# Performance work log

Measured on AMD Instinct MI355X. Metric: run time of the kernel, lower is better.

## Reference

```python
import jax, jax.numpy as jnp
import numpy as np

L, B, S, D, H = 6, 2, 2048, 512, 8
DH = D // H
FF = 4 * D
EPS = 1e-5


def setup_inputs() -> dict:
    key = jax.random.key(0)
    ks = jax.random.split(key, 10)
    w = lambda k, shape: jax.random.normal(k, shape, jnp.float32) * 0.02
    return {
        "query": jax.random.normal(ks[0], (B, S, D), jnp.float32),
        "key": jax.random.normal(ks[1], (B, S, D), jnp.float32),
        "query_mask": jnp.ones((B, S), jnp.int32),
        "key_mask": jnp.ones((B, S), jnp.int32),
        # per-layer stacked params; conv1d(kernel=1) == linear with weight [out,in]
        "Wq": w(ks[2], (L, D, D)), "bq": jnp.zeros((L, D), jnp.float32),
        "Wk": w(ks[3], (L, D, D)), "bk": jnp.zeros((L, D), jnp.float32),
        "Wv": w(ks[4], (L, D, D)), "bv": jnp.zeros((L, D), jnp.float32),
        "Wo": w(ks[5], (L, D, D)), "bo": jnp.zeros((L, D), jnp.float32),
        "ln1_g": jnp.ones((L, D), jnp.float32), "ln1_b": jnp.zeros((L, D), jnp.float32),
        "ff_w1": w(ks[6], (L, FF, D)), "ff_b1": jnp.zeros((L, FF), jnp.float32),
        "ff_w2": w(ks[7], (L, D, FF)), "ff_b2": jnp.zeros((L, D), jnp.float32),
        "ln2_g": jnp.ones((L, D), jnp.float32), "ln2_b": jnp.zeros((L, D), jnp.float32),
    }


def _layer_norm(x, g, b):
    m = jnp.mean(x, axis=-1, keepdims=True)
    v = jnp.mean(jnp.square(x - m), axis=-1, keepdims=True)
    return (x - m) * jax.lax.rsqrt(v + EPS) * g + b


def reference(query, key, query_mask, key_mask,
              Wq, bq, Wk, bk, Wv, bv, Wo, bo,
              ln1_g, ln1_b, ff_w1, ff_b1, ff_w2, ff_b2, ln2_g, ln2_b):
    b_, s_, d_ = query.shape
    kpad = (key_mask == 0)[:, None, None, :]          # [B,1,1,K]
    qm = query_mask.astype(query.dtype)[:, :, None]    # [B,S,1]
    x = query
    for i in range(L):
        # QKV projections (conv1d kernel-size-1 == linear), split heads -> [B,H,S,DH]
        def split(t):
            return t.reshape(b_, s_, H, DH).transpose(0, 2, 1, 3)
        q = split(x @ Wq[i].T + bq[i]) * (float(DH) ** -0.5)
        k = split(key @ Wk[i].T + bk[i])
        v = split(key @ Wv[i].T + bv[i])
        attn = jnp.einsum('bhqd,bhkd->bhqk', q, k)
        attn = jnp.where(kpad, -jnp.inf, attn)
        attn = jax.nn.softmax(attn, axis=-1)
        o = jnp.einsum('bhqk,bhkd->bhqd', attn, v)
        o = o.transpose(0, 2, 1, 3).reshape(b_, s_, H * DH)
        o = (o @ Wo[i].T + bo[i]) * qm                 # output proj + query mask
        x = _layer_norm(o + x, ln1_g[i], ln1_b[i])
        h = jax.nn.leaky_relu(x @ ff_w1[i].T + ff_b1[i], 0.01)
        f = (h @ ff_w2[i].T + ff_b2[i]) * qm           # FFN mask on output
        x = _layer_norm(f + x, ln2_g[i], ln2_b[i])
    return x
```

## Files before the change

### kernel.cpp

```cpp
#include <hip/hip_runtime.h>
#include <stdint.h>

constexpr int LAYERS = 6;
constexpr int Bc = 2, Sc = 2048, Dc = 512, Hc = 8, DHc = 64, FFc = 2048;
constexpr int Mc = Bc * Sc;
constexpr int NS = 2;
constexpr int KCHUNK = Sc / NS;

typedef __attribute__((ext_vector_type(8))) __bf16 bf16x8;
typedef __attribute__((ext_vector_type(4))) __bf16 bf16x4;
typedef __attribute__((ext_vector_type(4))) float f32x4;

__device__ __forceinline__ void async_ld16(const void* g, void* lds) {
  __builtin_amdgcn_global_load_lds(
      (const __attribute__((address_space(1))) uint32_t*)g,
      (__attribute__((address_space(3))) uint32_t*)lds, 16, 0, 0);
}

__global__ __launch_bounds__(256) void cvt_kernel(const float* __restrict__ in,
                                                  __bf16* __restrict__ out, int n) {
  int i = (blockIdx.x * 256 + threadIdx.x) * 4;
  if (i + 4 > n) return;
  const float4 v = *(const float4*)(in + i);
  bf16x4 o;
  o[0] = (__bf16)v.x; o[1] = (__bf16)v.y; o[2] = (__bf16)v.z; o[3] = (__bf16)v.w;
  *(bf16x4*)(out + i) = o;
}

__global__ __launch_bounds__(256) void cvt_kv_kernel(const float* __restrict__ Wk,
                                                     const float* __restrict__ Wv,
                                                     __bf16* __restrict__ out) {
  size_t i = ((size_t)blockIdx.x * 256 + threadIdx.x) * 4;
  int n = (int)(i / ((size_t)Dc * Dc));
  int lyr = n >> 1, p = n & 1;
  size_t idx = i - (size_t)n * Dc * Dc;
  const float* src = (p ? Wv : Wk) + (size_t)lyr * Dc * Dc + idx;
  const float4 v = *(const float4*)src;
  bf16x4 o;
  o[0] = (__bf16)v.x; o[1] = (__bf16)v.y; o[2] = (__bf16)v.z; o[3] = (__bf16)v.w;
  *(bf16x4*)(out + i) = o;
}

__global__ __launch_bounds__(256) void kbias_kernel(const int* __restrict__ km,
                                                    float* __restrict__ kb, int n) {
  int i = blockIdx.x * 256 + threadIdx.x;
  if (i < n) kb[i] = km[i] ? 0.f : -1e30f;
}

template <int BM, int BN, int WM, int WN, int EPI>
__global__ __launch_bounds__(256) void gemm_bt(
    const __bf16* __restrict__ A, const __bf16* __restrict__ W,
    const float* __restrict__ bias, const float* __restrict__ bias2,
    float* __restrict__ outf, __bf16* __restrict__ outb,
    __bf16* __restrict__ outb2, float scale,
    int M, int N, int K, int Kstride) {
  constexpr int BK = 64;
  __shared__ __bf16 As[2][BM * BK];
  __shared__ __bf16 Bs[2][BN * BK];
  const int tid = threadIdx.x;
  const int l15 = tid & 15;
  const int lg = (tid & 63) >> 4;
  const int w = tid >> 6;
  const int wm = w >> 1, wn = w & 1;
  const int tm = blockIdx.y * BM;
  const int tn = blockIdx.x * BN;
  const int z = blockIdx.z;
  const __bf16* Ap = A + (size_t)tm * Kstride + (size_t)z * K;
  const __bf16* Wp = W + (size_t)tn * Kstride + (size_t)z * K;
  f32x4 acc[WM][WN] = {};

  auto stage = [&](int k0, int bf) {
#pragma unroll
    for (int c = 0; c < BM * 8 / 256; ++c) {
      int cc = c * 256 + tid;
      int r = cc >> 3, s = cc & 7;
      int ss = s ^ (r & 7);
      async_ld16(Ap + (size_t)r * Kstride + k0 + ss * 8, &As[bf][cc * 8]);
    }
#pragma unroll
    for (int c = 0; c < BN * 8 / 256; ++c) {
      int cc = c * 256 + tid;
      int r = cc >> 3, s = cc & 7;
      int ss = s ^ (r & 7);
      async_ld16(Wp + (size_t)r * Kstride + k0 + ss * 8, &Bs[bf][cc * 8]);
    }
  };

  const int nk = K / BK;
  stage(0, 0);
  __syncthreads();
  int buf = 0;
  for (int t = 0; t < nk; ++t) {
    if (t + 1 < nk) stage((t + 1) * BK, buf ^ 1);
    bf16x8 af[WM][2], bfr[WN][2];
#pragma unroll
    for (int i = 0; i < WM; ++i) {
      int row = wm * WM * 16 + i * 16 + l15;
#pragma unroll
      for (int kf = 0; kf < 2; ++kf)
        af[i][kf] = *(const bf16x8*)&As[buf][row * 64 + (((kf * 4 + lg) ^ (row & 7)) * 8)];
    }
#pragma unroll
    for (int j = 0; j < WN; ++j) {
      int row = wn * WN * 16 + j * 16 + l15;
#pragma unroll
      for (int kf = 0; kf < 2; ++kf)
        bfr[j][kf] = *(const bf16x8*)&Bs[buf][row * 64 + (((kf * 4 + lg) ^ (row & 7)) * 8)];
    }
#pragma unroll
    for (int kf = 0; kf < 2; ++kf)
#pragma unroll
      for (int i = 0; i < WM; ++i)
#pragma unroll
        for (int j = 0; j < WN; ++j)
          acc[i][j] = __builtin_amdgcn_mfma_f32_16x16x32_bf16(af[i][kf], bfr[j][kf], acc[i][j], 0, 0, 0);
    __syncthreads();
    buf ^= 1;
  }

  if constexpr (EPI == 6) {
    const bool isV = ((tn & 1023) >= 512);
    const int lyr = tn >> 10;
    const int b = tm >> 11;
    const int sbase = tm & (Sc - 1);
    if (isV) {
      __bf16* T = (__bf16*)&As[0][0];
#pragma unroll
      for (int i = 0; i < WM; ++i) {
#pragma unroll
        for (int j = 0; j < WN; ++j) {
          const int d = wn * WN * 16 + j * 16 + l15;
          const int dg = (tn & 511) + d;
          const float bv = bias2[lyr * 512 + dg];
          const int s0 = wm * WM * 16 + i * 16 + lg * 4;
          bf16x4 pk;
#pragma unroll
          for (int r = 0; r < 4; ++r) pk[r] = (__bf16)(acc[i][j][r] + bv);
          const int slot = (s0 >> 3) ^ (d & 7);
          *(bf16x4*)&T[d * 64 + slot * 8 + (s0 & 7)] = pk;
        }
      }
      __syncthreads();
      const int rr = tid >> 3;
      const int c8 = tid & 7;
#pragma unroll
      for (int pass = 0; pass < 4; ++pass) {
        const int d = pass * 32 + rr;
        const int slot = c8 ^ (d & 7);
        bf16x8 v8 = *(const bf16x8*)&T[d * 64 + slot * 8];
        const int dg = (tn & 511) + d;
        const int h = dg >> 6, dh = dg & 63;
        *(bf16x8*)&outb2[((((size_t)(lyr * Bc + b) * Hc + h)) * DHc + dh) * Sc +
                         sbase + c8 * 8] = v8;
      }
    } else {
#pragma unroll
      for (int i = 0; i < WM; ++i) {
#pragma unroll
        for (int j = 0; j < WN; ++j) {
          const int d = wn * WN * 16 + j * 16 + l15;
          const int dg = (tn & 511) + d;
          const float bv = bias[lyr * 512 + dg];
          const int h = dg >> 6, dh = dg & 63;
#pragma unroll
          for (int r = 0; r < 4; ++r) {
            const int s = sbase + wm * WM * 16 + i * 16 + lg * 4 + r;
            outb[((((size_t)(lyr * Bc + b) * Hc + h)) * Sc + s) * DHc + dh] =
                (__bf16)(acc[i][j][r] + bv);
          }
        }
      }
    }
    return;
  }

#pragma unroll
  for (int i = 0; i < WM; ++i) {
#pragma unroll
    for (int j = 0; j < WN; ++j) {
      const int n = tn + wn * WN * 16 + j * 16 + l15;
      float bv;
      if constexpr (EPI == 0) {
        bv = (z == 0) ? bias[n] : 0.f;
      } else {
        bv = bias[n];
      }
#pragma unroll
      for (int r = 0; r < 4; ++r) {
        const int m = tm + wm * WM * 16 + i * 16 + lg * 4 + r;
        float v = acc[i][j][r] + bv;
        if constexpr (EPI == 0) {
          outf[(size_t)z * M * N + (size_t)m * N + n] = v;
        } else if constexpr (EPI == 1) {
          int b = m >> 11, s = m & (Sc - 1);
          int h = n >> 6, dh = n & 63;
          outb[(((size_t)(b * Hc + h)) * Sc + s) * DHc + dh] = (__bf16)(v * scale);
        } else if constexpr (EPI == 4) {
          float lv = v > 0.f ? v : 0.01f * v;
          outb[(size_t)m * N + n] = (__bf16)lv;
        }
      }
    }
  }
}

__global__ __launch_bounds__(256, 5) void attn_kernel(
    const __bf16* __restrict__ q, const __bf16* __restrict__ k,
    const __bf16* __restrict__ vt, const float* __restrict__ kb,
    __bf16* __restrict__ Opart, float* __restrict__ mpart,
    float* __restrict__ lpart) {
  const int bid = blockIdx.x;
  const int o = (bid & 7) * 128 + (bid >> 3);
  const int qb = o & 31;
  const int p = o >> 5;
  const int bh = p >> 1;
  const int z = p & 1;
  const int b = bh >> 3;
  const int w = threadIdx.x >> 6;
  const int l = threadIdx.x & 63;
  const int l15 = l & 15;
  const int lg = l >> 4;
  const int tid = threadIdx.x;
  const int qbase = qb * 64 + w * 16;
  const int k0 = z * KCHUNK;

  const __bf16* qp = q + ((size_t)bh * Sc + qbase) * DHc;
  const __bf16* kp = k + (size_t)bh * Sc * DHc;
  const __bf16* vp = vt + (size_t)bh * DHc * Sc;
  const float* kbp = kb + (size_t)b * Sc;

  bf16x8 qf[2];
  qf[0] = *(const bf16x8*)(qp + l15 * DHc + lg * 8);
  qf[1] = *(const bf16x8*)(qp + l15 * DHc + 32 + lg * 8);

  bf16x8 onesf;
#pragma unroll
  for (int i = 0; i < 8; ++i) onesf[i] = (__bf16)1.0f;

  f32x4 oacc[4] = {};
  f32x4 lacc = {};
  float mr = -1e30f;

  __shared__ __bf16 Ks[2][4096];
  __shared__ __bf16 Vs[2][4096];

  auto stage = [&](int t, int bf) {
    const int kt = k0 + t * 64;
#pragma unroll
    for (int ii = 0; ii < 2; ++ii) {
      int i = ii * 256 + tid;
      int r = i >> 3;
      int bsrc = (i & 7) ^ (r & 7);
      async_ld16(kp + (size_t)(kt + r) * DHc + bsrc * 8, &Ks[bf][i * 8]);
      async_ld16(vp + (size_t)r * Sc + kt + bsrc * 8, &Vs[bf][i * 8]);
    }
  };

  stage(0, 0);
  __syncthreads();

  constexpr int NT = KCHUNK / 64;
  int buf = 0;
  for (int t = 0; t < NT; ++t) {
    const int kt = k0 + t * 64;
    if (t + 1 < NT) stage(t + 1, buf ^ 1);

    float4 mb4[4];
#pragma unroll
    for (int cb = 0; cb < 4; ++cb)
      mb4[cb] = *(const float4*)&kbp[kt + cb * 16 + lg * 4];

    f32x4 sacc[4] = {};
#pragma unroll
    for (int kf = 0; kf < 2; ++kf) {
#pragma unroll
      for (int cb = 0; cb < 4; ++cb) {
        int row = cb * 16 + l15;
        bf16x8 kfr = *(const bf16x8*)&Ks[buf][row * 64 + (((kf * 4 + lg) ^ (row & 7)) * 8)];
        sacc[cb] = __builtin_amdgcn_mfma_f32_16x16x32_bf16(kfr, qf[kf], sacc[cb], 0, 0, 0);
      }
    }
    sacc[0][0] += mb4[0].x; sacc[0][1] += mb4[0].y; sacc[0][2] += mb4[0].z; sacc[0][3] += mb4[0].w;
    sacc[1][0] += mb4[1].x; sacc[1][1] += mb4[1].y; sacc[1][2] += mb4[1].z; sacc[1][3] += mb4[1].w;
    sacc[2][0] += mb4[2].x; sacc[2][1] += mb4[2].y; sacc[2][2] += mb4[2].z; sacc[2][3] += mb4[2].w;
    sacc[3][0] += mb4[3].x; sacc[3][1] += mb4[3].y; sacc[3][2] += mb4[3].z; sacc[3][3] += mb4[3].w;

    float mx = sacc[0][0];
#pragma unroll
    for (int cb = 0; cb < 4; ++cb)
#pragma unroll
      for (int r = 0; r < 4; ++r) mx = fmaxf(mx, sacc[cb][r]);
    mx = fmaxf(mx, __shfl_xor(mx, 16, 64));
    mx = fmaxf(mx, __shfl_xor(mx, 32, 64));

    if (__any(mx > mr + 8.f)) {
      float mn = fmaxf(mr, mx);
      float f = __expf(mr - mn);
      mr = mn;
      float fj[4];
#pragma unroll
      for (int j = 0; j < 4; ++j) fj[j] = __shfl(f, lg * 4 + j, 64);
#pragma unroll
      for (int j = 0; j < 4; ++j) lacc[j] *= fj[j];
#pragma unroll
      for (int db = 0; db < 4; ++db)
#pragma unroll
        for (int j = 0; j < 4; ++j) oacc[db][j] *= fj[j];
    }

    unsigned pw[4][2];
#pragma unroll
    for (int cb = 0; cb < 4; ++cb) {
#pragma unroll
      for (int w2 = 0; w2 < 2; ++w2) {
        union { __bf16 h[2]; unsigned u; } cu;
        cu.h[0] = (__bf16)__expf(sacc[cb][2 * w2] - mr);
        cu.h[1] = (__bf16)__expf(sacc[cb][2 * w2 + 1] - mr);
        pw[cb][w2] = cu.u;
      }
    }

    const int srcA = ((lg & 1) * 2) * 16 + l15;
    const int srcB = srcA + 16;
    const bool hi = (lg >> 1) & 1;
#pragma unroll
    for (int kf = 0; kf < 2; ++kf) {
      unsigned t0a = __shfl((int)pw[kf * 2][0], srcA, 64);
      unsigned t0b = __shfl((int)pw[kf * 2 + 1][0], srcA, 64);
      unsigned t1a = __shfl((int)pw[kf * 2][1], srcA, 64);
      unsigned t1b = __shfl((int)pw[kf * 2 + 1][1], srcA, 64);
      unsigned t2a = __shfl((int)pw[kf * 2][0], srcB, 64);
      unsigned t2b = __shfl((int)pw[kf * 2 + 1][0], srcB, 64);
      unsigned t3a = __shfl((int)pw[kf * 2][1], srcB, 64);
      unsigned t3b = __shfl((int)pw[kf * 2 + 1][1], srcB, 64);
      union { unsigned u[4]; bf16x8 v; } pa;
      pa.u[0] = hi ? t0b : t0a;
      pa.u[1] = hi ? t1b : t1a;
      pa.u[2] = hi ? t2b : t2a;
      pa.u[3] = hi ? t3b : t3a;
      lacc = __builtin_amdgcn_mfma_f32_16x16x32_bf16(pa.v, onesf, lacc, 0, 0, 0);
#pragma unroll
      for (int db = 0; db < 4; ++db) {
        int row = db * 16 + l15;
        bf16x8 vf = *(const bf16x8*)&Vs[buf][row * 64 + (((kf * 4 + lg) ^ (row & 7)) * 8)];
        oacc[db] = __builtin_amdgcn_mfma_f32_16x16x32_bf16(pa.v, vf, oacc[db], 0, 0, 0);
      }
    }
    __syncthreads();
    buf ^= 1;
  }

  const size_t obase = (((size_t)(z * Bc * Hc + bh)) * Sc + qbase) * DHc;
#pragma unroll
  for (int db = 0; db < 4; ++db)
#pragma unroll
    for (int j = 0; j < 4; ++j)
      Opart[obase + (size_t)(lg * 4 + j) * DHc + db * 16 + l15] = (__bf16)oacc[db][j];
  const int row0 = (z * Bc * Hc + bh) * Sc + qbase;
  if (lg == 0) mpart[row0 + l15] = mr;
  if (l15 == 0) {
#pragma unroll
    for (int j = 0; j < 4; ++j) lpart[row0 + lg * 4 + j] = lacc[j];
  }
}

__global__ __launch_bounds__(256) void attn_combine(
    const __bf16* __restrict__ Opart, const float* __restrict__ mpart,
    const float* __restrict__ lpart, __bf16* __restrict__ out) {
  int t = blockIdx.x * 256 + threadIdx.x;
  int d = t & 63;
  int row = t >> 6;
  int bh = row >> 11, s = row & (Sc - 1);
  constexpr int RSTRIDE = Bc * Hc * Sc;
  float m0 = mpart[row], m1 = mpart[RSTRIDE + row];
  float l0 = lpart[row], l1 = lpart[RSTRIDE + row];
  float M = fmaxf(m0, m1);
  float e0 = __expf(m0 - M), e1 = __expf(m1 - M);
  float denom = e0 * l0 + e1 * l1;
  float o0 = (float)Opart[(size_t)row * DHc + d];
  float o1 = (float)Opart[((size_t)RSTRIDE + row) * DHc + d];
  float o = (e0 * o0 + e1 * o1) / denom;
  int b = bh >> 3, h = bh & 7;
  out[(((size_t)b * Sc + s)) * Dc + h * DHc + d] = (__bf16)o;
}

__global__ __launch_bounds__(256) void add_ln_kernel(
    const float* __restrict__ res, const float* __restrict__ res2,
    const int* __restrict__ rmask, const float* __restrict__ xin,
    const float* __restrict__ g, const float* __restrict__ bb,
    float* __restrict__ xo, __bf16* __restrict__ xbo) {
  const int row = blockIdx.x;
  const int tid = threadIdx.x;
  const float* rp = res + (size_t)row * Dc;
  const float* xp = xin + (size_t)row * Dc;
  float mfac = rmask ? (float)rmask[row] : 1.f;
  float a0 = rp[tid], a1 = rp[tid + 256];
  if (res2) {
    const float* r2p = res2 + (size_t)row * Dc;
    a0 += r2p[tid];
    a1 += r2p[tid + 256];
  }
  float v0 = a0 * mfac + xp[tid];
  float v1 = a1 * mfac + xp[tid + 256];
  float s = v0 + v1;
#pragma unroll
  for (int d = 1; d < 64; d <<= 1) s += __shfl_xor(s, d, 64);
  __shared__ float red[4], red2[4];
  if ((tid & 63) == 0) red[tid >> 6] = s;
  __syncthreads();
  float mean = (red[0] + red[1] + red[2] + red[3]) * (1.0f / Dc);
  float d0 = v0 - mean, d1 = v1 - mean;
  float qq = d0 * d0 + d1 * d1;
#pragma unroll
  for (int d = 1; d < 64; d <<= 1) qq += __shfl_xor(qq, d, 64);
  if ((tid & 63) == 0) red2[tid >> 6] = qq;
  __syncthreads();
  float var = (red2[0] + red2[1] + red2[2] + red2[3]) * (1.0f / Dc);
  float rs = rsqrtf(var + 1e-5f);
  float o0 = d0 * rs * g[tid] + bb[tid];
  float o1 = d1 * rs * g[tid + 256] + bb[tid + 256];
  xo[(size_t)row * Dc + tid] = o0;
  xo[(size_t)row * Dc + tid + 256] = o1;
  xbo[(size_t)row * Dc + tid] = (__bf16)o0;
  xbo[(size_t)row * Dc + tid + 256] = (__bf16)o1;
}

extern "C" void kernel_launch(void* const* d_in, const int* in_sizes, int n_in,
                              void* d_out, int out_size, void* d_ws, size_t ws_size,
                              hipStream_t stream) {
  (void)in_sizes; (void)n_in; (void)out_size; (void)ws_size;
  const float* query = (const float*)d_in[0];
  const float* key   = (const float*)d_in[1];
  const int* qmask   = (const int*)d_in[2];
  const int* kmask   = (const int*)d_in[3];
  const float* Wq = (const float*)d_in[4];
  const float* bq = (const float*)d_in[5];
  const float* Wk = (const float*)d_in[6];
  const float* bk = (const float*)d_in[7];
  const float* Wv = (const float*)d_in[8];
  const float* bv = (const float*)d_in[9];
  const float* Wo = (const float*)d_in[10];
  const float* bo = (const float*)d_in[11];
  const float* ln1g = (const float*)d_in[12];
  const float* ln1b = (const float*)d_in[13];
  const float* fw1 = (const float*)d_in[14];
  const float* fb1 = (const float*)d_in[15];
  const float* fw2 = (const float*)d_in[16];
  const float* fb2 = (const float*)d_in[17];
  const float* ln2g = (const float*)d_in[18];
  const float* ln2b = (const float*)d_in[19];

  char* ws = (char*)d_ws;
  size_t off = 0;
  auto carve = [&](size_t bytes) -> void* {
    void* p = ws + off;
    off += (bytes + 255) & ~(size_t)255;
    return p;
  };
  float* x_f    = (float*)carve((size_t)Mc * Dc * 4);
  float* tmp_f  = (float*)carve((size_t)2 * Mc * Dc * 4);
  __bf16* x_b   = (__bf16*)carve((size_t)Mc * Dc * 2);
  __bf16* key_b = (__bf16*)carve((size_t)Mc * Dc * 2);
  __bf16* q_b   = (__bf16*)carve((size_t)Mc * Dc * 2);
  __bf16* at_b  = (__bf16*)carve((size_t)Mc * Dc * 2);
  __bf16* h_b   = (__bf16*)carve((size_t)Mc * FFc * 2);
  __bf16* k_all = (__bf16*)carve((size_t)LAYERS * Mc * Dc * 2);
  __bf16* vt_all= (__bf16*)carve((size_t)LAYERS * Mc * Dc * 2);
  __bf16* wq_b  = (__bf16*)carve((size_t)LAYERS * Dc * Dc * 2);
  __bf16* wkv_b = (__bf16*)carve((size_t)LAYERS * 2 * Dc * Dc * 2);
  __bf16* wo_b  = (__bf16*)carve((size_t)LAYERS * Dc * Dc * 2);
  __bf16* w1_b  = (__bf16*)carve((size_t)LAYERS * FFc * Dc * 2);
  __bf16* w2_b  = (__bf16*)carve((size_t)LAYERS * Dc * FFc * 2);
  float* ml_f   = (float*)carve((size_t)NS * Bc * Hc * Sc * 4 * 2);
  float* kb_f   = (float*)carve((size_t)Bc * Sc * 4);

  __bf16* opart_b = h_b;
  float* mpart_f = ml_f;
  float* lpart_f = ml_f + (size_t)NS * Bc * Hc * Sc;
  float* tmp2_f = tmp_f + (size_t)Mc * Dc;

  auto cvt = [&](const float* src, __bf16* dst, int n) {
    cvt_kernel<<<n / 1024, 256, 0, stream>>>(src, dst, n);
  };
  cvt(query, x_b, Mc * Dc);
  cvt(key, key_b, Mc * Dc);
  cvt(Wq, wq_b, LAYERS * Dc * Dc);
  cvt_kv_kernel<<<LAYERS * 2 * Dc * Dc / 1024, 256, 0, stream>>>(Wk, Wv, wkv_b);
  cvt(Wo, wo_b, LAYERS * Dc * Dc);
  cvt(fw1, w1_b, LAYERS * FFc * Dc);
  cvt(fw2, w2_b, LAYERS * Dc * FFc);
  kbias_kernel<<<Bc * Sc / 256, 256, 0, stream>>>(kmask, kb_f, Bc * Sc);
  hipMemcpyAsync(x_f, query, (size_t)Mc * Dc * 4, hipMemcpyDeviceToDevice, stream);

  const dim3 blk(256);
  const dim3 gP64(Dc / 64, Mc / 64);
  const dim3 gOP(Dc / 64, Mc / 64, 2);
  const dim3 gFF2(Dc / 64, Mc / 64, 2);
  const dim3 gKV(LAYERS * 2 * Dc / 128, Mc / 64);
  const dim3 gFF1(FFc / 128, Mc / 64);
  const dim3 gAttn(Sc / 64 * Bc * Hc * NS);
  const dim3 gComb(Bc * Hc * Sc * DHc / 256);

  gemm_bt<64, 128, 2, 4, 6><<<gKV, blk, 0, stream>>>(
      key_b, wkv_b, bk, bv, nullptr, k_all, vt_all, 1.0f,
      Mc, LAYERS * 2 * Dc, Dc, Dc);

  for (int i = 0; i < LAYERS; ++i) {
    const __bf16* wq_i = wq_b + (size_t)i * Dc * Dc;
    const __bf16* wo_i = wo_b + (size_t)i * Dc * Dc;
    const __bf16* w1_i = w1_b + (size_t)i * FFc * Dc;
    const __bf16* w2_i = w2_b + (size_t)i * Dc * FFc;
    const __bf16* k_i  = k_all + (size_t)i * Mc * Dc;
    const __bf16* vt_i = vt_all + (size_t)i * Mc * Dc;

    gemm_bt<64, 64, 2, 2, 1><<<gP64, blk, 0, stream>>>(
        x_b, wq_i, bq + i * Dc, nullptr, nullptr, q_b, nullptr, 0.125f,
        Mc, Dc, Dc, Dc);
    attn_kernel<<<gAttn, blk, 0, stream>>>(q_b, k_i, vt_i, kb_f,
                                           opart_b, mpart_f, lpart_f);
    attn_combine<<<gComb, blk, 0, stream>>>(opart_b, mpart_f, lpart_f, at_b);
    gemm_bt<64, 64, 2, 2, 0><<<gOP, blk, 0, stream>>>(
        at_b, wo_i, bo + i * Dc, nullptr, tmp_f, nullptr, nullptr, 1.0f,
        Mc, Dc, Dc / 2, Dc);
    add_ln_kernel<<<Mc, blk, 0, stream>>>(tmp_f, tmp2_f, qmask, x_f,
                                          ln1g + i * Dc, ln1b + i * Dc, x_f, x_b);
    gemm_bt<64, 128, 2, 4, 4><<<gFF1, blk, 0, stream>>>(
        x_b, w1_i, fb1 + i * FFc, nullptr, nullptr, h_b, nullptr, 1.0f,
        Mc, FFc, Dc, Dc);
    gemm_bt<64, 64, 2, 2, 0><<<gFF2, blk, 0, stream>>>(
        h_b, w2_i, fb2 + i * Dc, nullptr, tmp_f, nullptr, nullptr, 1.0f,
        Mc, Dc, FFc / 2, FFc);
    add_ln_kernel<<<Mc, blk, 0, stream>>>(tmp_f, tmp2_f, qmask, x_f,
                                          ln2g + i * Dc, ln2b + i * Dc, x_f, x_b);
  }
  hipMemcpyAsync(d_out, x_f, (size_t)Mc * Dc * 4, hipMemcpyDeviceToDevice, stream);
}
```

Before: 815.4 us.

## Fuse conversion launches, vectorize add+LayerNorm, and raise MFMA wave priority in attention

Six separate fp32-to-bf16 conversion launches and the query memcpy are merged into one cvt_all kernel, which also writes the fp32 copy of x. The add+LayerNorm kernel now processes two rows per 256-thread block with float4 loads and stores, halving its grid and widening memory accesses. The attention kernel wraps its MFMA sections in s_setprio so waves issuing matrix ops get scheduling priority. The costs are a branchy index dispatch in the merged converter and the LayerNorm kernel no longer handling null res2 or rmask pointers.

```diff
diff --git a/kernel.cpp b/kernel.cpp
--- a/kernel.cpp
+++ b/kernel.cpp
@@ -17,14 +17,37 @@
       (__attribute__((address_space(3))) uint32_t*)lds, 16, 0, 0);
 }
 
-__global__ __launch_bounds__(256) void cvt_kernel(const float* __restrict__ in,
-                                                  __bf16* __restrict__ out, int n) {
-  int i = (blockIdx.x * 256 + threadIdx.x) * 4;
-  if (i + 4 > n) return;
-  const float4 v = *(const float4*)(in + i);
+__global__ __launch_bounds__(256) void cvt_all(
+    const float* __restrict__ Wq, const float* __restrict__ Wo,
+    const float* __restrict__ fw1, const float* __restrict__ fw2,
+    const float* __restrict__ query, const float* __restrict__ key,
+    __bf16* __restrict__ wq_b, __bf16* __restrict__ wo_b,
+    __bf16* __restrict__ w1_b, __bf16* __restrict__ w2_b,
+    __bf16* __restrict__ x_b, __bf16* __restrict__ key_b,
+    float* __restrict__ x_f) {
+  size_t i = ((size_t)blockIdx.x * 256 + threadIdx.x) * 4;
+  constexpr size_t nW = (size_t)LAYERS * Dc * Dc;
+  constexpr size_t nF = (size_t)LAYERS * FFc * Dc;
+  constexpr size_t nX = (size_t)Mc * Dc;
+  const float* src;
+  __bf16* dst;
+  float* fdst = nullptr;
+  if (i < nW) { src = Wq + i; dst = wq_b + i; }
+  else if (i < 2 * nW) { size_t j = i - nW; src = Wo + j; dst = wo_b + j; }
+  else if (i < 2 * nW + nF) { size_t j = i - 2 * nW; src = fw1 + j; dst = w1_b + j; }
+  else if (i < 2 * nW + 2 * nF) { size_t j = i - 2 * nW - nF; src = fw2 + j; dst = w2_b + j; }
+  else if (i < 2 * nW + 2 * nF + nX) {
+    size_t j = i - 2 * nW - 2 * nF;
+    src = query + j; dst = x_b + j; fdst = x_f + j;
+  } else {
+    size_t j = i - 2 * nW - 2 * nF - nX;
+    src = key + j; dst = key_b + j;
+  }
+  const float4 v = *(const float4*)src;
   bf16x4 o;
   o[0] = (__bf16)v.x; o[1] = (__bf16)v.y; o[2] = (__bf16)v.z; o[3] = (__bf16)v.w;
-  *(bf16x4*)(out + i) = o;
+  *(bf16x4*)dst = o;
+  if (fdst) *(float4*)fdst = v;
 }
 
 __global__ __launch_bounds__(256) void cvt_kv_kernel(const float* __restrict__ Wk,
@@ -271,6 +294,7 @@
       mb4[cb] = *(const float4*)&kbp[kt + cb * 16 + lg * 4];
 
     f32x4 sacc[4] = {};
+    __builtin_amdgcn_s_setprio(1);
 #pragma unroll
     for (int kf = 0; kf < 2; ++kf) {
 #pragma unroll
@@ -280,6 +304,7 @@
         sacc[cb] = __builtin_amdgcn_mfma_f32_16x16x32_bf16(kfr, qf[kf], sacc[cb], 0, 0, 0);
       }
     }
+    __builtin_amdgcn_s_setprio(0);
     sacc[0][0] += mb4[0].x; sacc[0][1] += mb4[0].y; sacc[0][2] += mb4[0].z; sacc[0][3] += mb4[0].w;
     sacc[1][0] += mb4[1].x; sacc[1][1] += mb4[1].y; sacc[1][2] += mb4[1].z; sacc[1][3] += mb4[1].w;
     sacc[2][0] += mb4[2].x; sacc[2][1] += mb4[2].y; sacc[2][2] += mb4[2].z; sacc[2][3] += mb4[2].w;
@@ -338,6 +363,7 @@
       pa.u[1] = hi ? t1b : t1a;
       pa.u[2] = hi ? t2b : t2a;
       pa.u[3] = hi ? t3b : t3a;
+      __builtin_amdgcn_s_setprio(1);
       lacc = __builtin_amdgcn_mfma_f32_16x16x32_bf16(pa.v, onesf, lacc, 0, 0, 0);
 #pragma unroll
       for (int db = 0; db < 4; ++db) {
@@ -345,6 +371,7 @@
         bf16x8 vf = *(const bf16x8*)&Vs[buf][row * 64 + (((kf * 4 + lg) ^ (row & 7)) * 8)];
         oacc[db] = __builtin_amdgcn_mfma_f32_16x16x32_bf16(pa.v, vf, oacc[db], 0, 0, 0);
       }
+      __builtin_amdgcn_s_setprio(0);
     }
     __syncthreads();
     buf ^= 1;
@@ -389,40 +416,47 @@
     const int* __restrict__ rmask, const float* __restrict__ xin,
     const float* __restrict__ g, const float* __restrict__ bb,
     float* __restrict__ xo, __bf16* __restrict__ xbo) {
-  const int row = blockIdx.x;
   const int tid = threadIdx.x;
-  const float* rp = res + (size_t)row * Dc;
-  const float* xp = xin + (size_t)row * Dc;
-  float mfac = rmask ? (float)rmask[row] : 1.f;
-  float a0 = rp[tid], a1 = rp[tid + 256];
-  if (res2) {
-    const float* r2p = res2 + (size_t)row * Dc;
-    a0 += r2p[tid];
-    a1 += r2p[tid + 256];
-  }
-  float v0 = a0 * mfac + xp[tid];
-  float v1 = a1 * mfac + xp[tid + 256];
-  float s = v0 + v1;
+  const int rl = tid >> 7;
+  const int row = blockIdx.x * 2 + rl;
+  const int ci = (tid & 127) * 4;
+  const size_t base = (size_t)row * Dc + ci;
+  const float4 a = *(const float4*)(res + base);
+  const float4 a2 = *(const float4*)(res2 + base);
+  const float4 xv = *(const float4*)(xin + base);
+  const float mfac = (float)rmask[row];
+  float4 v;
+  v.x = (a.x + a2.x) * mfac + xv.x;
+  v.y = (a.y + a2.y) * mfac + xv.y;
+  v.z = (a.z + a2.z) * mfac + xv.z;
+  v.w = (a.w + a2.w) * mfac + xv.w;
+  float s = v.x + v.y + v.z + v.w;
 #pragma unroll
   for (int d = 1; d < 64; d <<= 1) s += __shfl_xor(s, d, 64);
   __shared__ float red[4], red2[4];
   if ((tid & 63) == 0) red[tid >> 6] = s;
   __syncthreads();
-  float mean = (red[0] + red[1] + red[2] + red[3]) * (1.0f / Dc);
-  float d0 = v0 - mean, d1 = v1 - mean;
-  float qq = d0 * d0 + d1 * d1;
+  float mean = (red[rl * 2] + red[rl * 2 + 1]) * (1.0f / Dc);
+  float4 dv;
+  dv.x = v.x - mean; dv.y = v.y - mean; dv.z = v.z - mean; dv.w = v.w - mean;
+  float qq = dv.x * dv.x + dv.y * dv.y + dv.z * dv.z + dv.w * dv.w;
 #pragma unroll
   for (int d = 1; d < 64; d <<= 1) qq += __shfl_xor(qq, d, 64);
   if ((tid & 63) == 0) red2[tid >> 6] = qq;
   __syncthreads();
-  float var = (red2[0] + red2[1] + red2[2] + red2[3]) * (1.0f / Dc);
+  float var = (red2[rl * 2] + red2[rl * 2 + 1]) * (1.0f / Dc);
   float rs = rsqrtf(var + 1e-5f);
-  float o0 = d0 * rs * g[tid] + bb[tid];
-  float o1 = d1 * rs * g[tid + 256] + bb[tid + 256];
-  xo[(size_t)row * Dc + tid] = o0;
-  xo[(size_t)row * Dc + tid + 256] = o1;
-  xbo[(size_t)row * Dc + tid] = (__bf16)o0;
-  xbo[(size_t)row * Dc + tid + 256] = (__bf16)o1;
+  const float4 gv = *(const float4*)(g + ci);
+  const float4 bv = *(const float4*)(bb + ci);
+  float4 ov;
+  ov.x = dv.x * rs * gv.x + bv.x;
+  ov.y = dv.y * rs * gv.y + bv.y;
+  ov.z = dv.z * rs * gv.z + bv.z;
+  ov.w = dv.w * rs * gv.w + bv.w;
+  *(float4*)(xo + base) = ov;
+  bf16x4 ob;
+  ob[0] = (__bf16)ov.x; ob[1] = (__bf16)ov.y; ob[2] = (__bf16)ov.z; ob[3] = (__bf16)ov.w;
+  *(bf16x4*)(xbo + base) = ob;
 }
 
 extern "C" void kernel_launch(void* const* d_in, const int* in_sizes, int n_in,
@@ -479,18 +513,10 @@
   float* lpart_f = ml_f + (size_t)NS * Bc * Hc * Sc;
   float* tmp2_f = tmp_f + (size_t)Mc * Dc;
 
-  auto cvt = [&](const float* src, __bf16* dst, int n) {
-    cvt_kernel<<<n / 1024, 256, 0, stream>>>(src, dst, n);
-  };
-  cvt(query, x_b, Mc * Dc);
-  cvt(key, key_b, Mc * Dc);
-  cvt(Wq, wq_b, LAYERS * Dc * Dc);
+  cvt_all<<<19456, 256, 0, stream>>>(Wq, Wo, fw1, fw2, query, key,
+                                     wq_b, wo_b, w1_b, w2_b, x_b, key_b, x_f);
   cvt_kv_kernel<<<LAYERS * 2 * Dc * Dc / 1024, 256, 0, stream>>>(Wk, Wv, wkv_b);
-  cvt(Wo, wo_b, LAYERS * Dc * Dc);
-  cvt(fw1, w1_b, LAYERS * FFc * Dc);
-  cvt(fw2, w2_b, LAYERS * Dc * FFc);
   kbias_kernel<<<Bc * Sc / 256, 256, 0, stream>>>(kmask, kb_f, Bc * Sc);
-  hipMemcpyAsync(x_f, query, (size_t)Mc * Dc * 4, hipMemcpyDeviceToDevice, stream);
 
   const dim3 blk(256);
   const dim3 gP64(Dc / 64, Mc / 64);
@@ -500,6 +526,7 @@
   const dim3 gFF1(FFc / 128, Mc / 64);
   const dim3 gAttn(Sc / 64 * Bc * Hc * NS);
   const dim3 gComb(Bc * Hc * Sc * DHc / 256);
+  const dim3 gLN(Mc / 2);
 
   gemm_bt<64, 128, 2, 4, 6><<<gKV, blk, 0, stream>>>(
       key_b, wkv_b, bk, bv, nullptr, k_all, vt_all, 1.0f,
@@ -522,16 +549,16 @@
     gemm_bt<64, 64, 2, 2, 0><<<gOP, blk, 0, stream>>>(
         at_b, wo_i, bo + i * Dc, nullptr, tmp_f, nullptr, nullptr, 1.0f,
         Mc, Dc, Dc / 2, Dc);
-    add_ln_kernel<<<Mc, blk, 0, stream>>>(tmp_f, tmp2_f, qmask, x_f,
-                                          ln1g + i * Dc, ln1b + i * Dc, x_f, x_b);
+    add_ln_kernel<<<gLN, blk, 0, stream>>>(tmp_f, tmp2_f, qmask, x_f,
+                                           ln1g + i * Dc, ln1b + i * Dc, x_f, x_b);
     gemm_bt<64, 128, 2, 4, 4><<<gFF1, blk, 0, stream>>>(
         x_b, w1_i, fb1 + i * FFc, nullptr, nullptr, h_b, nullptr, 1.0f,
         Mc, FFc, Dc, Dc);
     gemm_bt<64, 64, 2, 2, 0><<<gFF2, blk, 0, stream>>>(
         h_b, w2_i, fb2 + i * Dc, nullptr, tmp_f, nullptr, nullptr, 1.0f,
         Mc, Dc, FFc / 2, FFc);
-    add_ln_kernel<<<Mc, blk, 0, stream>>>(tmp_f, tmp2_f, qmask, x_f,
-                                          ln2g + i * Dc, ln2b + i * Dc, x_f, x_b);
+    add_ln_kernel<<<gLN, blk, 0, stream>>>(tmp_f, tmp2_f, qmask, x_f,
+                                           ln2g + i * Dc, ln2b + i * Dc, x_f, x_b);
   }
   hipMemcpyAsync(d_out, x_f, (size_t)Mc * Dc * 4, hipMemcpyDeviceToDevice, stream);
 }
```

Measured after the change: 789.2 us. 3.2% less time.
